# Performance work log

Hardware: AMD Instinct MI355X
Metric: run time of the kernel (lower is better)

## Reference

```python
import jax, jax.numpy as jnp
import numpy as np

N, E, G = 50000, 800000, 512
DIN, HID, DOUT, L, DE = 64, 64, 128, 3, 16
NEG_SLOPE = 0.2
BN_EPS = 1e-5


def setup_inputs() -> dict:
    key = jax.random.key(0)
    ks = jax.random.split(key, 20)
    s = 0.1  # weight scale for numerical stability
    return {
        "x": jax.random.normal(ks[0], (N, DIN), jnp.float32),
        "edge_index": jax.random.randint(ks[1], (2, E), 0, N, jnp.int32),
        "edge_attr": jax.random.normal(ks[2], (E, DE), jnp.float32),
        "batch": jnp.sort(jax.random.randint(ks[3], (N,), 0, G, jnp.int32)),
        "emb_W": jax.random.normal(ks[4], (HID, DIN), jnp.float32) * s,
        "emb_b": jax.random.normal(ks[5], (HID,), jnp.float32) * s,
        "Wl": jax.random.normal(ks[6], (L, HID, HID), jnp.float32) * s,
        "bl": jax.random.normal(ks[7], (L, HID), jnp.float32) * s,
        "Wr": jax.random.normal(ks[8], (L, HID, HID), jnp.float32) * s,
        "br": jax.random.normal(ks[9], (L, HID), jnp.float32) * s,
        "We": jax.random.normal(ks[10], (L, HID, DE), jnp.float32) * s,
        "att": jax.random.normal(ks[11], (L, HID), jnp.float32) * s,
        "conv_bias": jax.random.normal(ks[12], (L, HID), jnp.float32) * s,
        "bn_gamma": jax.random.uniform(ks[13], (L, HID), jnp.float32, 0.5, 1.5),
        "bn_beta": jax.random.normal(ks[14], (L, HID), jnp.float32) * s,
        "bn_mean": jnp.zeros((L, HID), jnp.float32),
        "bn_var": jnp.ones((L, HID), jnp.float32),
        "lin_W": jax.random.normal(ks[15], (DOUT, HID), jnp.float32) * s,
        "lin_b": jax.random.normal(ks[16], (DOUT,), jnp.float32) * s,
    }


def _gatv2(h, src, dst, edge_attr, Wl, bl, Wr, br, We, att, bias):
    # GATv2Conv, heads=1, concat=False, with edge features
    xl = h @ Wl.T + bl                      # [N,C] source transform (also message value)
    xr = h @ Wr.T + br                      # [N,C] target transform
    ea = edge_attr @ We.T                   # [E,C]
    m = xl[src] + xr[dst] + ea              # [E,C]
    m = jax.nn.leaky_relu(m, NEG_SLOPE)
    alpha = m @ att                         # [E] attention logits
    amax = jax.ops.segment_max(alpha, dst, num_segments=N)
    ea_exp = jnp.exp(alpha - amax[dst])
    denom = jax.ops.segment_sum(ea_exp, dst, num_segments=N)
    alpha = ea_exp / (denom[dst] + 1e-16)
    out = jax.ops.segment_sum(alpha[:, None] * xl[src], dst, num_segments=N)
    return out + bias


def reference(x, edge_index, edge_attr, batch, emb_W, emb_b, Wl, bl, Wr, br,
              We, att, conv_bias, bn_gamma, bn_beta, bn_mean, bn_var, lin_W, lin_b):
    src, dst = edge_index[0], edge_index[1]
    h = x @ emb_W.T + emb_b
    for i in range(L):
        hc = _gatv2(h, src, dst, edge_attr, Wl[i], bl[i], Wr[i], br[i],
                    We[i], att[i], conv_bias[i])
        # BatchNorm (eval mode, running stats)
        hc = (hc - bn_mean[i]) * jax.lax.rsqrt(bn_var[i] + BN_EPS) * bn_gamma[i] + bn_beta[i]
        hc = jax.nn.gelu(hc, approximate=False)  # torch F.gelu default is exact erf
        h = h + hc                                # residual; dropout p=0 / eval -> identity
    out = h @ lin_W.T + lin_b                     # [N,DOUT]
    counts = jax.ops.segment_sum(jnp.ones((N,), out.dtype), batch, num_segments=G)
    pooled = jax.ops.segment_sum(out, batch, num_segments=G)
    return pooled / jnp.maximum(counts, 1.0)[:, None]
```

## Files before the change

kernel.cpp:

```cpp
#include <hip/hip_runtime.h>
#include <math.h>

#define NEG_SLOPE 0.2f
#define BN_EPS 1e-5f

template <int N> struct IC { static constexpr int v = N; };
template <bool B> struct BC { static constexpr bool v = B; };

typedef _Float16 half2v __attribute__((ext_vector_type(2)));
typedef _Float16 f16x8 __attribute__((ext_vector_type(8)));
typedef float f32x4v __attribute__((ext_vector_type(4)));

__device__ __forceinline__ half2v u2h(unsigned u) {
  union { unsigned u; half2v h; } c;
  c.u = u;
  return c.h;
}
__device__ __forceinline__ unsigned pkh(float lo, float hi) {
  union { half2v h; unsigned u; } c;
  c.h[0] = (_Float16)lo;
  c.h[1] = (_Float16)hi;
  return c.u;
}

#if defined(__has_builtin)
#if __has_builtin(__builtin_amdgcn_fdot2)
#define FDOT2(a, b, c) __builtin_amdgcn_fdot2((a), (b), (c), false)
#endif
#endif
#ifndef FDOT2
__device__ __forceinline__ float fdot2_sw(half2v a, half2v b, float c) {
  return c + (float)a[0] * (float)b[0] + (float)a[1] * (float)b[1];
}
#define FDOT2(a, b, c) fdot2_sw((a), (b), (c))
#endif

#if defined(__has_builtin)
#if __has_builtin(__builtin_amdgcn_exp2f)
#define FEXP(x) __builtin_amdgcn_exp2f(x)
#define ATT_SCALE 1.44269504088896f
#endif
#endif
#ifndef FEXP
#define FEXP(x) __expf(x)
#define ATT_SCALE 1.0f
#endif

#define FMA4(acc, v, wq) \
  acc += (v).x * (wq).x + (v).y * (wq).y + (v).z * (wq).z + (v).w * (wq).w

#define DOT_ROW(buf, r, bias, OUT)                                     \
  {                                                                    \
    __builtin_amdgcn_sched_barrier(0);                                 \
    float a0 = 0.f, a1 = 0.f, a2 = 0.f, a3 = 0.f;                      \
    _Pragma("unroll") for (int q = 0; q < 4; q++) {                    \
      float4 v0 = *(const float4*)((buf) + (r) * 64 + q * 16 + 0);     \
      float4 v1 = *(const float4*)((buf) + (r) * 64 + q * 16 + 4);     \
      float4 v2 = *(const float4*)((buf) + (r) * 64 + q * 16 + 8);     \
      float4 v3 = *(const float4*)((buf) + (r) * 64 + q * 16 + 12);    \
      FMA4(a0, v0, W[q * 4 + 0]);                                      \
      FMA4(a1, v1, W[q * 4 + 1]);                                      \
      FMA4(a2, v2, W[q * 4 + 2]);                                      \
      FMA4(a3, v3, W[q * 4 + 3]);                                      \
    }                                                                  \
    OUT = (bias) + ((a0 + a1) + (a2 + a3));                            \
  }

__device__ __forceinline__ float wave_sum64(float v) {
  int x;
  x = __builtin_amdgcn_update_dpp(0, __float_as_int(v), 0x121, 0xF, 0xF, true);
  v += __int_as_float(x);
  x = __builtin_amdgcn_update_dpp(0, __float_as_int(v), 0x122, 0xF, 0xF, true);
  v += __int_as_float(x);
  x = __builtin_amdgcn_update_dpp(0, __float_as_int(v), 0x124, 0xF, 0xF, true);
  v += __int_as_float(x);
  x = __builtin_amdgcn_update_dpp(0, __float_as_int(v), 0x128, 0xF, 0xF, true);
  v += __int_as_float(x);
  x = __builtin_amdgcn_update_dpp(0, __float_as_int(v), 0x142, 0xF, 0xF, true);
  v += __int_as_float(x);
  x = __builtin_amdgcn_update_dpp(0, __float_as_int(v), 0x143, 0xF, 0xF, true);
  v += __int_as_float(x);
  return __int_as_float(__builtin_amdgcn_readlane(__float_as_int(v), 63));
}

__global__ __launch_bounds__(256) void hist_kernel(
    const int* __restrict__ dst, const int* __restrict__ batch,
    int* __restrict__ deg, float* __restrict__ counts, int E_, int N_) {
  int i = blockIdx.x * 256 + threadIdx.x;
  if (i < E_) atomicAdd(&deg[dst[i]], 1);
  if (i < N_) atomicAdd(&counts[batch[i]], 1.0f);
}

__global__ __launch_bounds__(256) void scanA_kernel(
    const int* __restrict__ deg, int* __restrict__ row_ptr,
    int* __restrict__ segTot, int N_, int nseg) {
  __shared__ int sb[256];
  int t = threadIdx.x;
  for (int s = blockIdx.x; s < nseg; s += gridDim.x) {
    int i = s * 256 + t;
    int v = (i < N_) ? deg[i] : 0;
    sb[t] = v;
    __syncthreads();
    for (int off = 1; off < 256; off <<= 1) {
      int a = (t >= off) ? sb[t - off] : 0;
      __syncthreads();
      sb[t] += a;
      __syncthreads();
    }
    int incl = sb[t];
    if (i < N_) row_ptr[i] = incl - v;
    if (t == 255) segTot[s] = incl;
    __syncthreads();
  }
}

__global__ __launch_bounds__(256) void scanB_kernel(int* __restrict__ segTot,
                                                    int nseg) {
  __shared__ int sb[256];
  __shared__ int baseSh;
  int t = threadIdx.x;
  if (t == 0) baseSh = 0;
  __syncthreads();
  for (int c0 = 0; c0 < nseg; c0 += 256) {
    int s = c0 + t;
    int v = (s < nseg) ? segTot[s] : 0;
    sb[t] = v;
    __syncthreads();
    for (int off = 1; off < 256; off <<= 1) {
      int a = (t >= off) ? sb[t - off] : 0;
      __syncthreads();
      sb[t] += a;
      __syncthreads();
    }
    int incl = sb[t];
    int base = baseSh;
    if (s < nseg) segTot[s] = base + incl - v;
    __syncthreads();
    if (t == 255) baseSh = base + incl;
    __syncthreads();
  }
}

__global__ __launch_bounds__(256) void scanC_kernel(
    int* __restrict__ row_ptr, const int* __restrict__ segTot,
    int* __restrict__ cursor, int N_, int E_) {
  int tid = blockIdx.x * 256 + threadIdx.x;
  int nt = gridDim.x * 256;
  for (int i = tid; i < N_; i += nt) {
    int rp = row_ptr[i] + segTot[i >> 8];
    row_ptr[i] = rp;
    cursor[i] = rp;
  }
  if (tid == 0) row_ptr[N_] = E_;
}

__global__ __launch_bounds__(256) void scatter_kernel(
    const int* __restrict__ src, const int* __restrict__ dst,
    int* __restrict__ cursor, int* __restrict__ csr_src,
    int* __restrict__ csr_eid, int E_) {
  int e = blockIdx.x * 256 + threadIdx.x;
  if (e >= E_) return;
  int pos = atomicAdd(&cursor[dst[e]], 1);
  csr_src[pos] = src[e];
  csr_eid[pos] = e;
}

__global__ __launch_bounds__(256) void permute_attr_kernel(
    const float4* __restrict__ edge_attr4, const int* __restrict__ csr_eid,
    unsigned* __restrict__ attr_u, int E_) {
  int p = blockIdx.x * 256 + threadIdx.x;
  if (p >= E_) return;
  int e = csr_eid[p];
  float4 a0 = edge_attr4[(size_t)e * 4 + 0];
  float4 a1 = edge_attr4[(size_t)e * 4 + 1];
  float4 a2 = edge_attr4[(size_t)e * 4 + 2];
  float4 a3 = edge_attr4[(size_t)e * 4 + 3];
  uint4 u0, u1;
  u0.x = pkh(a0.x, a0.y);
  u0.y = pkh(a0.z, a0.w);
  u0.z = pkh(a1.x, a1.y);
  u0.w = pkh(a1.z, a1.w);
  u1.x = pkh(a2.x, a2.y);
  u1.y = pkh(a2.z, a2.w);
  u1.z = pkh(a3.x, a3.y);
  u1.w = pkh(a3.z, a3.w);
  uint4* d4 = (uint4*)(attr_u + (size_t)p * 8);
  d4[0] = u0;
  d4[1] = u1;
}

__global__ __launch_bounds__(256) void pack_w16_kernel(
    const float* __restrict__ Wl, const float* __restrict__ Wr,
    _Float16* __restrict__ w16, int per) {
  int i = blockIdx.x * 256 + threadIdx.x;
  if (i < per) {
    w16[i] = (_Float16)Wl[i];
  } else if (i < 2 * per) {
    w16[i] = (_Float16)Wr[i - per];
  }
}

__global__ __launch_bounds__(256, 3) void emb_kernel(
    const float* __restrict__ x, const float* __restrict__ emb_W,
    const float* __restrict__ emb_b, float* __restrict__ h, int rows) {
  __shared__ float sx[4096];
  int lane = threadIdx.x & 63;
  int w = threadIdx.x >> 6;
  int n0 = blockIdx.x * 64;

  {
    int gmax = rows * 64 - 4;
#pragma unroll
    for (int i = 0; i < 4; i++) {
      int off = w * 1024 + i * 256 + lane * 4;
      int g = min(n0 * 64 + off, gmax);
      *(float4*)(sx + off) = *(const float4*)(x + g);
    }
  }

  float4 W[16];
#pragma unroll
  for (int q = 0; q < 16; q++) W[q] = ((const float4*)(emb_W + lane * 64))[q];
  float b = emb_b[lane];
#pragma unroll 1
  for (int t = 0; t < 16; t++) {
    int r = w * 16 + t;
    float a;
    DOT_ROW(sx, r, b, a);
    int n = n0 + r;
    if (n < rows) h[(size_t)n * 64 + lane] = a;
  }
}

#if defined(__has_builtin)
#if __has_builtin(__builtin_amdgcn_mfma_f32_16x16x32_f16)
#define HAVE_MFMA16 1
#endif
#endif

__global__ __launch_bounds__(256) void linx_mfma_kernel(
    const float* __restrict__ in, const _Float16* __restrict__ Wl16,
    const float* __restrict__ bl, const _Float16* __restrict__ Wr16,
    const float* __restrict__ br, _Float16* __restrict__ xl,
    _Float16* __restrict__ xr, int rows) {
#ifdef HAVE_MFMA16
  int lane = threadIdx.x & 63;
  int w = threadIdx.x >> 6;
  int n0 = blockIdx.x * 64 + w * 16;
  int r = lane & 15;
  int kg = lane >> 4;

  int nA = min(n0 + r, rows - 1);
  f16x8 A0, A1;
  {
    const float* p = in + (size_t)nA * 64 + kg * 8;
    float4 xa = *(const float4*)(p);
    float4 xb = *(const float4*)(p + 4);
    A0[0] = (_Float16)xa.x; A0[1] = (_Float16)xa.y;
    A0[2] = (_Float16)xa.z; A0[3] = (_Float16)xa.w;
    A0[4] = (_Float16)xb.x; A0[5] = (_Float16)xb.y;
    A0[6] = (_Float16)xb.z; A0[7] = (_Float16)xb.w;
    xa = *(const float4*)(p + 32);
    xb = *(const float4*)(p + 36);
    A1[0] = (_Float16)xa.x; A1[1] = (_Float16)xa.y;
    A1[2] = (_Float16)xa.z; A1[3] = (_Float16)xa.w;
    A1[4] = (_Float16)xb.x; A1[5] = (_Float16)xb.y;
    A1[6] = (_Float16)xb.z; A1[7] = (_Float16)xb.w;
  }

#pragma unroll
  for (int c = 0; c < 4; c++) {
    int o = c * 16 + r;
    {
      const f16x8* b0 = (const f16x8*)(Wl16 + (size_t)o * 64 + kg * 8);
      const f16x8* b1 = (const f16x8*)(Wl16 + (size_t)o * 64 + 32 + kg * 8);
      f32x4v acc;
      float bv = bl[o];
      acc[0] = bv; acc[1] = bv; acc[2] = bv; acc[3] = bv;
      acc = __builtin_amdgcn_mfma_f32_16x16x32_f16(A0, b0[0], acc, 0, 0, 0);
      acc = __builtin_amdgcn_mfma_f32_16x16x32_f16(A1, b1[0], acc, 0, 0, 0);
#pragma unroll
      for (int g = 0; g < 4; g++) {
        int nd = n0 + kg * 4 + g;
        if (nd < rows) xl[(size_t)nd * 64 + o] = (_Float16)acc[g];
      }
    }
    {
      const f16x8* b0 = (const f16x8*)(Wr16 + (size_t)o * 64 + kg * 8);
      const f16x8* b1 = (const f16x8*)(Wr16 + (size_t)o * 64 + 32 + kg * 8);
      f32x4v acc;
      float bv = br[o];
      acc[0] = bv; acc[1] = bv; acc[2] = bv; acc[3] = bv;
      acc = __builtin_amdgcn_mfma_f32_16x16x32_f16(A0, b0[0], acc, 0, 0, 0);
      acc = __builtin_amdgcn_mfma_f32_16x16x32_f16(A1, b1[0], acc, 0, 0, 0);
#pragma unroll
      for (int g = 0; g < 4; g++) {
        int nd = n0 + kg * 4 + g;
        if (nd < rows) xr[(size_t)nd * 64 + o] = (_Float16)acc[g];
      }
    }
  }
#endif
}

template <bool CONTIG>
__global__ __launch_bounds__(256) void gat_fused_kernel(
    const int* __restrict__ csr_src, const int* __restrict__ csr_eid,
    const int* __restrict__ row_ptr, const unsigned* __restrict__ attr_u,
    const float* __restrict__ edge_attr, const _Float16* __restrict__ xl,
    const _Float16* __restrict__ xr, const float* __restrict__ We,
    const float* __restrict__ att, const float* __restrict__ conv_bias,
    const float* __restrict__ gamma, const float* __restrict__ beta,
    const float* __restrict__ mean, const float* __restrict__ var,
    float* __restrict__ h, int N_) {
  int d = (blockIdx.x * 256 + threadIdx.x) >> 6;
  if (d >= N_) return;
  int j = threadIdx.x & 63;
  half2v Wek2[8];
  float Wekf[16];
  if constexpr (CONTIG) {
#pragma unroll
    for (int q = 0; q < 8; q++) {
      Wek2[q][0] = (_Float16)We[j * 16 + 2 * q];
      Wek2[q][1] = (_Float16)We[j * 16 + 2 * q + 1];
    }
  } else {
#pragma unroll
    for (int k = 0; k < 16; k++) Wekf[k] = We[j * 16 + k];
  }
  float att_j = att[j] * ATT_SCALE;
  float sc = rsqrtf(var[j] + BN_EPS) * gamma[j];
  float sh = (conv_bias[j] - mean[j]) * sc + beta[j];

  int beg = __builtin_amdgcn_readfirstlane(row_ptr[d]);
  int end = __builtin_amdgcn_readfirstlane(row_ptr[d + 1]);
  float xrj = (float)xr[(size_t)d * 64 + j];
  float m = -INFINITY, l = 0.f, acc = 0.f;

  auto chunk = [&](int base, auto C_, auto PAD_) {
    constexpr int C = decltype(C_)::v;
    constexpr bool PAD = decltype(PAD_)::v;
    int si[C];
#pragma unroll
    for (int t = 0; t < C; t++) {
      int idx = PAD ? min(base + t, end - 1) : (base + t);
      si[t] = csr_src[idx];
    }
    float xlv[C];
#pragma unroll
    for (int t = 0; t < C; t++)
      xlv[t] = (float)xl[(size_t)si[t] * 64 + j];
    float v[C];
#pragma unroll
    for (int t = 0; t < C; t++) {
      int idx = PAD ? min(base + t, end - 1) : (base + t);
      float ea;
      if constexpr (CONTIG) {
        const uint4* ap = (const uint4*)(attr_u + (size_t)idx * 8);
        uint4 ua = ap[0], ub = ap[1];
        ea = 0.f;
        ea = FDOT2(u2h(ua.x), Wek2[0], ea);
        ea = FDOT2(u2h(ua.y), Wek2[1], ea);
        ea = FDOT2(u2h(ua.z), Wek2[2], ea);
        ea = FDOT2(u2h(ua.w), Wek2[3], ea);
        ea = FDOT2(u2h(ub.x), Wek2[4], ea);
        ea = FDOT2(u2h(ub.y), Wek2[5], ea);
        ea = FDOT2(u2h(ub.z), Wek2[6], ea);
        ea = FDOT2(u2h(ub.w), Wek2[7], ea);
      } else {
        const float4* ap =
            (const float4*)(edge_attr + (size_t)csr_eid[idx] * 16);
        float4 a0 = ap[0], a1 = ap[1], a2 = ap[2], a3 = ap[3];
        ea = a0.x * Wekf[0]  + a0.y * Wekf[1]  + a0.z * Wekf[2]  + a0.w * Wekf[3]
           + a1.x * Wekf[4]  + a1.y * Wekf[5]  + a1.z * Wekf[6]  + a1.w * Wekf[7]
           + a2.x * Wekf[8]  + a2.y * Wekf[9]  + a2.z * Wekf[10] + a2.w * Wekf[11]
           + a3.x * Wekf[12] + a3.y * Wekf[13] + a3.z * Wekf[14] + a3.w * Wekf[15];
      }
      float z = xlv[t] + xrj + ea;
      z = fmaxf(z, NEG_SLOPE * z);
      float p = wave_sum64(z * att_j);
      v[t] = (!PAD || (base + t < end)) ? p : -INFINITY;
    }
    float mc = v[0];
#pragma unroll
    for (int t = 1; t < C; t++) mc = fmaxf(mc, v[t]);
    float newm = fmaxf(m, mc);
    float s = FEXP(m - newm);
    l *= s;
    acc *= s;
#pragma unroll
    for (int t = 0; t < C; t++) {
      float w = FEXP(v[t] - newm);
      l += w;
      acc += w * xlv[t];
    }
    m = newm;
  };

  int base = beg;
  for (; base + 16 <= end; base += 16) chunk(base, IC<16>{}, BC<false>{});
  if (base + 8 <= end) {
    chunk(base, IC<8>{}, BC<false>{});
    base += 8;
  }
  if (base < end) chunk(base, IC<8>{}, BC<true>{});

  float val = acc / (l + 1e-16f) * sc + sh;
  float g = 0.5f * val * (1.f + erff(val * 0.70710678118654752f));
  h[(size_t)d * 64 + j] += g;
}

__global__ __launch_bounds__(256, 2) void lin_pool_kernel(
    const float* __restrict__ h, const float* __restrict__ lin_W,
    const float* __restrict__ lin_b, const int* __restrict__ batch,
    const float* __restrict__ counts, float* __restrict__ pooled, int rows) {
  __shared__ float shh[4096];
  int lane = threadIdx.x & 63;
  int w = threadIdx.x >> 6;
  int n0 = blockIdx.x * 64;

  {
    int gmax = rows * 64 - 4;
#pragma unroll
    for (int i = 0; i < 4; i++) {
      int off = w * 1024 + i * 256 + lane * 4;
      int g = min(n0 * 64 + off, gmax);
      *(float4*)(shh + off) = *(const float4*)(h + g);
    }
  }

  float4 W0[16], W1[16];
#pragma unroll
  for (int q = 0; q < 16; q++) W0[q] = ((const float4*)(lin_W + lane * 64))[q];
#pragma unroll
  for (int q = 0; q < 16; q++)
    W1[q] = ((const float4*)(lin_W + (lane + 64) * 64))[q];
  float b0 = lin_b[lane], b1 = lin_b[lane + 64];

  int curg = -1;
  float acc0 = 0.f, acc1 = 0.f;
  int lim = min(16, rows - n0 - w * 16);
#pragma unroll 1
  for (int t = 0; t < lim; t++) {
    int r = w * 16 + t;
    __builtin_amdgcn_sched_barrier(0);
    float d0 = b0, d1 = b1;
#pragma unroll
    for (int q = 0; q < 16; q++) {
      float4 v = *(const float4*)(shh + r * 64 + q * 4);
      FMA4(d0, v, W0[q]);
      FMA4(d1, v, W1[q]);
    }
    int g = batch[n0 + r];
    if (g != curg) {
      if (curg >= 0) {
        float inv = 1.f / fmaxf(counts[curg], 1.f);
        atomicAdd(&pooled[curg * 128 + lane], acc0 * inv);
        atomicAdd(&pooled[curg * 128 + 64 + lane], acc1 * inv);
      }
      curg = g;
      acc0 = 0.f;
      acc1 = 0.f;
    }
    acc0 += d0;
    acc1 += d1;
  }
  if (curg >= 0) {
    float inv = 1.f / fmaxf(counts[curg], 1.f);
    atomicAdd(&pooled[curg * 128 + lane], acc0 * inv);
    atomicAdd(&pooled[curg * 128 + 64 + lane], acc1 * inv);
  }
}

extern "C" void kernel_launch(void* const* d_in, const int* in_sizes, int n_in,
                              void* d_out, int out_size, void* d_ws, size_t ws_size,
                              hipStream_t stream) {
  const float* x         = (const float*)d_in[0];
  const int*   edge_index= (const int*)  d_in[1];
  const float* edge_attr = (const float*)d_in[2];
  const int*   batch     = (const int*)  d_in[3];
  const float* emb_W     = (const float*)d_in[4];
  const float* emb_b     = (const float*)d_in[5];
  const float* Wl        = (const float*)d_in[6];
  const float* bl        = (const float*)d_in[7];
  const float* Wr        = (const float*)d_in[8];
  const float* br        = (const float*)d_in[9];
  const float* We        = (const float*)d_in[10];
  const float* att       = (const float*)d_in[11];
  const float* conv_bias = (const float*)d_in[12];
  const float* bn_gamma  = (const float*)d_in[13];
  const float* bn_beta   = (const float*)d_in[14];
  const float* bn_mean   = (const float*)d_in[15];
  const float* bn_var    = (const float*)d_in[16];
  const float* lin_W     = (const float*)d_in[17];
  const float* lin_b     = (const float*)d_in[18];

  const int N_ = in_sizes[0] / 64;
  const int E_ = in_sizes[1] / 2;
  const int G_ = out_size / 128;
  const int* src = edge_index;
  const int* dst = edge_index + E_;

  const int Npad = (N_ + 3) & ~3;
  const int Epad = (E_ + 19) & ~3;
  const int nseg = (N_ + 255) / 256;

  float* ws      = (float*)d_ws;
  float* h       = ws;
  _Float16* xl   = (_Float16*)(h + (size_t)N_ * 64);
  _Float16* xr   = xl + (size_t)N_ * 64;
  int*   csr_src = (int*)(xr + (size_t)N_ * 64);
  int*   csr_eid = csr_src + Epad;
  int*   row_ptr = csr_eid + Epad;
  int*   cursor  = row_ptr + (Npad + 4);
  int*   deg     = cursor + Npad;
  float* counts  = (float*)(deg + Npad);
  int*   segTot  = (int*)(counts + G_);
  uintptr_t abp  = (uintptr_t)(segTot + nseg + 8);
  abp = (abp + 15) & ~(uintptr_t)15;
  _Float16* w16  = (_Float16*)abp;
  uintptr_t abp2 = abp + 24576 * sizeof(_Float16);
  unsigned* attr_u = (unsigned*)abp2;

  size_t base_bytes = (abp2 - (uintptr_t)d_ws);
  bool contig = ws_size >= base_bytes + (size_t)E_ * 32 + 64;

  const int hgrid = (max(E_, N_) + 255) / 256;
  const int ngrid = (N_ + 255) / 256;
  const int egrid = (E_ + 255) / 256;

  hipMemsetAsync(deg, 0, ((size_t)Npad + G_) * 4, stream);
  hist_kernel<<<hgrid, 256, 0, stream>>>(dst, batch, deg, counts, E_, N_);
  scanA_kernel<<<min(nseg, 1024), 256, 0, stream>>>(deg, row_ptr, segTot, N_,
                                                    nseg);
  scanB_kernel<<<1, 256, 0, stream>>>(segTot, nseg);
  scanC_kernel<<<ngrid, 256, 0, stream>>>(row_ptr, segTot, cursor, N_, E_);
  scatter_kernel<<<egrid, 256, 0, stream>>>(src, dst, cursor, csr_src,
                                            csr_eid, E_);
  if (contig) {
    permute_attr_kernel<<<egrid, 256, 0, stream>>>(
        (const float4*)edge_attr, csr_eid, attr_u, E_);
  }

  pack_w16_kernel<<<(24576 + 255) / 256, 256, 0, stream>>>(Wl, Wr, w16,
                                                           12288);
  const int tgrid = (N_ + 63) / 64;
  emb_kernel<<<tgrid, 256, 0, stream>>>(x, emb_W, emb_b, h, N_);

  const int gatBlocks = (N_ + 3) / 4;
  for (int l = 0; l < 3; l++) {
    linx_mfma_kernel<<<tgrid, 256, 0, stream>>>(
        h, w16 + (size_t)l * 4096, bl + l * 64, w16 + 12288 + (size_t)l * 4096,
        br + l * 64, xl, xr, N_);
    if (contig) {
      gat_fused_kernel<true><<<gatBlocks, 256, 0, stream>>>(
          csr_src, csr_eid, row_ptr, attr_u, edge_attr, xl, xr,
          We + (size_t)l * 1024, att + l * 64, conv_bias + l * 64,
          bn_gamma + l * 64, bn_beta + l * 64, bn_mean + l * 64,
          bn_var + l * 64, h, N_);
    } else {
      gat_fused_kernel<false><<<gatBlocks, 256, 0, stream>>>(
          csr_src, csr_eid, row_ptr, attr_u, edge_attr, xl, xr,
          We + (size_t)l * 1024, att + l * 64, conv_bias + l * 64,
          bn_gamma + l * 64, bn_beta + l * 64, bn_mean + l * 64,
          bn_var + l * 64, h, N_);
    }
  }

  hipMemsetAsync(d_out, 0, (size_t)G_ * 128 * 4, stream);
  lin_pool_kernel<<<(N_ + 63) / 64, 256, 0, stream>>>(
      h, lin_W, lin_b, batch, counts, (float*)d_out, N_);
}
```

Before: 564.9 us.

## Schedule GAT destination nodes by descending degree via counting-sort permutation

Adds a degree histogram, a scan and a scatter that build a permutation of destination nodes sorted by in-degree, highest first, reusing the deg buffer. The GAT kernel then maps each wave to a permuted node, so waves in a block have similar edge counts and the heaviest nodes start early. It also makes the source indices wave-uniform with readfirstlane and adds a 4-edge tail chunk so short tails pad less. The cost is three extra small kernels plus a memset, and writes to h become scattered rather than in node order.

```diff
diff --git a/kernel.cpp b/kernel.cpp
--- a/kernel.cpp
+++ b/kernel.cpp
@@ -152,6 +152,41 @@
     cursor[i] = rp;
   }
   if (tid == 0) row_ptr[N_] = E_;
+}
+
+__global__ __launch_bounds__(256) void dhist_kernel(
+    const int* __restrict__ row_ptr, int* __restrict__ bins, int N_) {
+  int i = blockIdx.x * 256 + threadIdx.x;
+  if (i < N_) {
+    int dg = row_ptr[i + 1] - row_ptr[i];
+    atomicAdd(&bins[127 - min(dg, 127)], 1);
+  }
+}
+
+__global__ __launch_bounds__(128) void dscan_kernel(int* __restrict__ bins) {
+  __shared__ int sb[128];
+  int t = threadIdx.x;
+  int v = bins[t];
+  sb[t] = v;
+  __syncthreads();
+  for (int off = 1; off < 128; off <<= 1) {
+    int a = (t >= off) ? sb[t - off] : 0;
+    __syncthreads();
+    sb[t] += a;
+    __syncthreads();
+  }
+  bins[t] = sb[t] - v;
+}
+
+__global__ __launch_bounds__(256) void dscatter_kernel(
+    const int* __restrict__ row_ptr, int* __restrict__ bins,
+    int* __restrict__ perm, int N_) {
+  int i = blockIdx.x * 256 + threadIdx.x;
+  if (i < N_) {
+    int dg = row_ptr[i + 1] - row_ptr[i];
+    int pos = atomicAdd(&bins[127 - min(dg, 127)], 1);
+    perm[pos] = i;
+  }
 }
 
 __global__ __launch_bounds__(256) void scatter_kernel(
@@ -305,16 +340,17 @@
 
 template <bool CONTIG>
 __global__ __launch_bounds__(256) void gat_fused_kernel(
-    const int* __restrict__ csr_src, const int* __restrict__ csr_eid,
-    const int* __restrict__ row_ptr, const unsigned* __restrict__ attr_u,
-    const float* __restrict__ edge_attr, const _Float16* __restrict__ xl,
-    const _Float16* __restrict__ xr, const float* __restrict__ We,
-    const float* __restrict__ att, const float* __restrict__ conv_bias,
-    const float* __restrict__ gamma, const float* __restrict__ beta,
-    const float* __restrict__ mean, const float* __restrict__ var,
-    float* __restrict__ h, int N_) {
-  int d = (blockIdx.x * 256 + threadIdx.x) >> 6;
-  if (d >= N_) return;
+    const int* __restrict__ perm, const int* __restrict__ csr_src,
+    const int* __restrict__ csr_eid, const int* __restrict__ row_ptr,
+    const unsigned* __restrict__ attr_u, const float* __restrict__ edge_attr,
+    const _Float16* __restrict__ xl, const _Float16* __restrict__ xr,
+    const float* __restrict__ We, const float* __restrict__ att,
+    const float* __restrict__ conv_bias, const float* __restrict__ gamma,
+    const float* __restrict__ beta, const float* __restrict__ mean,
+    const float* __restrict__ var, float* __restrict__ h, int N_) {
+  int widx = (blockIdx.x * 256 + threadIdx.x) >> 6;
+  if (widx >= N_) return;
+  int d = __builtin_amdgcn_readfirstlane(perm[widx]);
   int j = threadIdx.x & 63;
   half2v Wek2[8];
   float Wekf[16];
@@ -344,7 +380,7 @@
 #pragma unroll
     for (int t = 0; t < C; t++) {
       int idx = PAD ? min(base + t, end - 1) : (base + t);
-      si[t] = csr_src[idx];
+      si[t] = __builtin_amdgcn_readfirstlane(csr_src[idx]);
     }
     float xlv[C];
 #pragma unroll
@@ -403,7 +439,11 @@
     chunk(base, IC<8>{}, BC<false>{});
     base += 8;
   }
-  if (base < end) chunk(base, IC<8>{}, BC<true>{});
+  if (base + 4 <= end) {
+    chunk(base, IC<4>{}, BC<false>{});
+    base += 4;
+  }
+  if (base < end) chunk(base, IC<4>{}, BC<true>{});
 
   float val = acc / (l + 1e-16f) * sc + sh;
   float g = 0.5f * val * (1.f + erff(val * 0.70710678118654752f));
@@ -516,11 +556,13 @@
   int*   deg     = cursor + Npad;
   float* counts  = (float*)(deg + Npad);
   int*   segTot  = (int*)(counts + G_);
-  uintptr_t abp  = (uintptr_t)(segTot + nseg + 8);
+  int*   bins    = segTot + nseg + 8;
+  uintptr_t abp  = (uintptr_t)(bins + 128);
   abp = (abp + 15) & ~(uintptr_t)15;
   _Float16* w16  = (_Float16*)abp;
   uintptr_t abp2 = abp + 24576 * sizeof(_Float16);
   unsigned* attr_u = (unsigned*)abp2;
+  int* perm = deg;
 
   size_t base_bytes = (abp2 - (uintptr_t)d_ws);
   bool contig = ws_size >= base_bytes + (size_t)E_ * 32 + 64;
@@ -537,6 +579,10 @@
   scanC_kernel<<<ngrid, 256, 0, stream>>>(row_ptr, segTot, cursor, N_, E_);
   scatter_kernel<<<egrid, 256, 0, stream>>>(src, dst, cursor, csr_src,
                                             csr_eid, E_);
+  hipMemsetAsync(bins, 0, 128 * 4, stream);
+  dhist_kernel<<<ngrid, 256, 0, stream>>>(row_ptr, bins, N_);
+  dscan_kernel<<<1, 128, 0, stream>>>(bins);
+  dscatter_kernel<<<ngrid, 256, 0, stream>>>(row_ptr, bins, perm, N_);
   if (contig) {
     permute_attr_kernel<<<egrid, 256, 0, stream>>>(
         (const float4*)edge_attr, csr_eid, attr_u, E_);
@@ -554,13 +600,13 @@
         br + l * 64, xl, xr, N_);
     if (contig) {
       gat_fused_kernel<true><<<gatBlocks, 256, 0, stream>>>(
-          csr_src, csr_eid, row_ptr, attr_u, edge_attr, xl, xr,
+          perm, csr_src, csr_eid, row_ptr, attr_u, edge_attr, xl, xr,
           We + (size_t)l * 1024, att + l * 64, conv_bias + l * 64,
           bn_gamma + l * 64, bn_beta + l * 64, bn_mean + l * 64,
           bn_var + l * 64, h, N_);
     } else {
       gat_fused_kernel<false><<<gatBlocks, 256, 0, stream>>>(
-          csr_src, csr_eid, row_ptr, attr_u, edge_attr, xl, xr,
+          perm, csr_src, csr_eid, row_ptr, attr_u, edge_attr, xl, xr,
           We + (size_t)l * 1024, att + l * 64, conv_bias + l * 64,
           bn_gamma + l * 64, bn_beta + l * 64, bn_mean + l * 64,
           bn_var + l * 64, h, N_);
```

New measurement: 820.5 us. 45.2% more time.
